# Optimization experiments

Hardware: AMD Instinct MI355X
Metric: run time of the kernel (lower is better)

## Reference

```python
import jax, jax.numpy as jnp
import numpy as np

DIM = 384
KERNEL = 31
PAD = KERNEL // 2


def setup_inputs() -> dict:
    key = jax.random.key(0)
    k1, k2 = jax.random.split(key)
    x = jax.random.normal(k1, (32, DIM, 56, 56), dtype=jnp.float32)
    weight = jax.random.normal(k2, (DIM, 1, KERNEL, KERNEL), dtype=jnp.float32)
    bias_term = jnp.zeros((DIM,), dtype=jnp.float32)
    return {"x": x, "weight": weight, "bias_term": bias_term}


def reference(x, weight, bias_term):
    # Depthwise conv2d: groups == channels, stride 1, SAME-style padding k//2.
    out = jax.lax.conv_general_dilated(
        x, weight,
        window_strides=(1, 1),
        padding=[(PAD, PAD), (PAD, PAD)],
        dimension_numbers=("NCHW", "OIHW", "NCHW"),
        feature_group_count=DIM,
    )
    return out + bias_term[None, :, None, None]
```

## Files before the change

kernel.cpp:

```cpp
#include <hip/hip_runtime.h>


#define DIMC 384
#define HW 56
#define KS 31
#define PADK 15
#define TILE 86
#define LDS_STRIDE 88
#define RH 14
#define XR (RH + KS - 1)

__global__ __launch_bounds__(256, 4)
void dwconv31_kernel(const float* __restrict__ x,
                     const float* __restrict__ w,
                     const float* __restrict__ bias,
                     float* __restrict__ out)
{
    __shared__ float tile[TILE * LDS_STRIDE];

    const int plane = blockIdx.x;
    const int c = plane % DIMC;
    const float* __restrict__ xp = x + (size_t)plane * (HW * HW);
    const float* __restrict__ wp = w + (size_t)c * (KS * KS);
    const int tid = threadIdx.x;

    for (int idx = tid; idx < TILE * TILE; idx += 256) {
        int r  = idx / TILE;
        int cc = idx - r * TILE;
        int gr = r - PADK;
        int gc = cc - PADK;
        float v = 0.0f;
        if ((unsigned)gr < (unsigned)HW && (unsigned)gc < (unsigned)HW)
            v = xp[gr * HW + gc];
        tile[r * LDS_STRIDE + cc] = v;
    }
    __syncthreads();

    const int tx = tid & 63;
    const int h0 = (tid >> 6) * RH;

    float acc[RH];
#pragma unroll
    for (int j = 0; j < RH; ++j) acc[j] = 0.0f;

    if (tx < HW) {
#pragma unroll 1
        for (int kw = 0; kw < KS; ++kw) {
            float xr[XR];
#pragma unroll
            for (int i = 0; i < XR; ++i)
                xr[i] = tile[(h0 + i) * LDS_STRIDE + tx + kw];

#pragma unroll
            for (int kh = 0; kh < KS; ++kh) {
                float wv = wp[kh * KS + kw];
#pragma unroll
                for (int j = 0; j < RH; ++j)
                    acc[j] = fmaf(xr[j + kh], wv, acc[j]);
            }
        }

        const float b = bias[c];
        float* __restrict__ op = out + (size_t)plane * (HW * HW);
#pragma unroll
        for (int j = 0; j < RH; ++j)
            op[(h0 + j) * HW + tx] = acc[j] + b;
    }
}

extern "C" void kernel_launch(void* const* d_in, const int* in_sizes, int n_in,
                              void* d_out, int out_size, void* d_ws, size_t ws_size,
                              hipStream_t stream) {
    const float* x    = (const float*)d_in[0];
    const float* wgt  = (const float*)d_in[1];
    const float* bias = (const float*)d_in[2];
    float* out = (float*)d_out;

    const int nplanes = 32 * DIMC;
    dwconv31_kernel<<<nplanes, 256, 0, stream>>>(x, wgt, bias, out);
}
```

Measured before the change: 975.9 us.

## Use fp16 packed dot2 with shifted LDS tiles for depthwise conv

Converts the input tile and weights to fp16 in shared memory and computes the 31x31 depthwise convolution with v_dot2 instructions, which handle two kw taps per instruction while accumulating in fp32. A second tile shifted by one column keeps the half2 loads aligned for odd output columns, and the weights are prepacked as pairs in LDS. This roughly halves the arithmetic instruction count, at the cost of fp16 rounding of inputs and weights, which may exceed tolerance given the 961-term sums.

```diff
diff --git a/kernel.cpp b/kernel.cpp
--- a/kernel.cpp
+++ b/kernel.cpp
@@ -5,18 +5,30 @@
 #define HW 56
 #define KS 31
 #define PADK 15
-#define TILE 86
-#define LDS_STRIDE 88
+#define TROWS 86
+#define TCOLS 88
 #define RH 14
-#define XR (RH + KS - 1)
+#define NP 16
+
+typedef _Float16 half2v __attribute__((ext_vector_type(2)));
+
+__device__ __forceinline__ float dot2f(half2v a, half2v b, float c) {
+#if defined(__has_builtin) && __has_builtin(__builtin_amdgcn_fdot2)
+    return __builtin_amdgcn_fdot2(a, b, c, false);
+#else
+    return fmaf((float)a.x, (float)b.x, fmaf((float)a.y, (float)b.y, c));
+#endif
+}
 
 __global__ __launch_bounds__(256, 4)
-void dwconv31_kernel(const float* __restrict__ x,
-                     const float* __restrict__ w,
-                     const float* __restrict__ bias,
-                     float* __restrict__ out)
+void dwconv31_dot2(const float* __restrict__ x,
+                   const float* __restrict__ w,
+                   const float* __restrict__ bias,
+                   float* __restrict__ out)
 {
-    __shared__ float tile[TILE * LDS_STRIDE];
+    __shared__ _Float16 t0[TROWS * TCOLS];
+    __shared__ _Float16 t1[TROWS * TCOLS];
+    __shared__ half2v  wlds[KS * NP];
 
     const int plane = blockIdx.x;
     const int c = plane % DIMC;
@@ -24,15 +36,28 @@
     const float* __restrict__ wp = w + (size_t)c * (KS * KS);
     const int tid = threadIdx.x;
 
-    for (int idx = tid; idx < TILE * TILE; idx += 256) {
-        int r  = idx / TILE;
-        int cc = idx - r * TILE;
+    for (int i = tid; i < KS * NP; i += 256) {
+        int kh = i / NP, p = i - kh * NP;
+        float a = wp[kh * KS + 2 * p];
+        float b = (2 * p + 1 < KS) ? wp[kh * KS + 2 * p + 1] : 0.0f;
+        half2v hv;
+        hv.x = (_Float16)a;
+        hv.y = (_Float16)b;
+        wlds[i] = hv;
+    }
+
+    for (int idx = tid; idx < TROWS * TCOLS; idx += 256) {
+        int r  = idx / TCOLS;
+        int cc = idx - r * TCOLS;
         int gr = r - PADK;
         int gc = cc - PADK;
         float v = 0.0f;
         if ((unsigned)gr < (unsigned)HW && (unsigned)gc < (unsigned)HW)
             v = xp[gr * HW + gc];
-        tile[r * LDS_STRIDE + cc] = v;
+        _Float16 hv = (_Float16)v;
+        t0[r * TCOLS + cc] = hv;
+        if (cc >= 1) t1[r * TCOLS + cc - 1] = hv;
+        else         t1[r * TCOLS + TCOLS - 1] = (_Float16)0.0f;
     }
     __syncthreads();
 
@@ -44,19 +69,30 @@
     for (int j = 0; j < RH; ++j) acc[j] = 0.0f;
 
     if (tx < HW) {
+        const _Float16* base = (tx & 1) ? (t1 + (tx - 1)) : (t0 + tx);
+
 #pragma unroll 1
-        for (int kw = 0; kw < KS; ++kw) {
-            float xr[XR];
+        for (int p = 0; p < NP; ++p) {
+            const _Float16* colp = base + 2 * p;
+#pragma unroll 1
+            for (int khc = 0; khc < 2; ++khc) {
+                const int kh0 = khc * 16;
+                const int nkh = khc ? 15 : 16;
+
+                half2v xr[29];
 #pragma unroll
-            for (int i = 0; i < XR; ++i)
-                xr[i] = tile[(h0 + i) * LDS_STRIDE + tx + kw];
+                for (int i = 0; i < 29; ++i)
+                    xr[i] = *(const half2v*)(colp + (h0 + kh0 + i) * TCOLS);
 
 #pragma unroll
-            for (int kh = 0; kh < KS; ++kh) {
-                float wv = wp[kh * KS + kw];
+                for (int kk = 0; kk < 16; ++kk) {
+                    if (kk < nkh) {
+                        half2v wv = wlds[(kh0 + kk) * NP + p];
 #pragma unroll
-                for (int j = 0; j < RH; ++j)
-                    acc[j] = fmaf(xr[j + kh], wv, acc[j]);
+                        for (int j = 0; j < RH; ++j)
+                            acc[j] = dot2f(xr[kk + j], wv, acc[j]);
+                    }
+                }
             }
         }
 
@@ -77,5 +113,5 @@
     float* out = (float*)d_out;
 
     const int nplanes = 32 * DIMC;
-    dwconv31_kernel<<<nplanes, 256, 0, stream>>>(x, wgt, bias, out);
+    dwconv31_dot2<<<nplanes, 256, 0, stream>>>(x, wgt, bias, out);
 }
```

Measured after the change: 913.7 us. 1.07x faster.
